# Performance work log

Measured on AMD Instinct MI355X. Metric: run time of the kernel, lower is better.

## Reference

```python
import jax, jax.numpy as jnp
import numpy as np

OUT_FEATURES = 4096
IN_FEATURES = 4096
GROUP_SIZE = 64
N_GROUPS = OUT_FEATURES * IN_FEATURES // GROUP_SIZE  # 262144


def setup_inputs() -> dict:
    key = jax.random.key(0)
    ks = jax.random.split(key, 8)
    x = jax.random.normal(ks[0], (4, 2048, IN_FEATURES), dtype=jnp.float32)
    W_q = jax.random.randint(ks[1], (N_GROUPS, GROUP_SIZE), 0, 16, dtype=jnp.int32)
    scale_q = jax.random.randint(ks[2], (N_GROUPS,), 0, 256, dtype=jnp.int32)
    zero_q = jax.random.randint(ks[3], (N_GROUPS,), 0, 256, dtype=jnp.int32)
    # meta for the nested (quantized) scale / zero: affine params
    s_scale = jax.random.uniform(ks[4], (1,), dtype=jnp.float32) * 1e-3 + 1e-4
    z_scale = jax.random.uniform(ks[5], (1,), dtype=jnp.float32) * 8.0
    s_zero = jax.random.uniform(ks[6], (1,), dtype=jnp.float32) * 0.1 + 1e-3
    z_zero = jax.random.uniform(ks[7], (1,), dtype=jnp.float32) * 8.0
    bias = jax.random.normal(jax.random.fold_in(key, 99), (OUT_FEATURES,), dtype=jnp.float32)
    return {"x": x, "W_q": W_q, "scale_q": scale_q, "zero_q": zero_q,
            "s_scale": s_scale, "z_scale": z_scale,
            "s_zero": s_zero, "z_zero": z_zero, "bias": bias}


def _dequantize(W_q, scale_q, zero_q, s_scale, z_scale, s_zero, z_zero):
    # Nested dequant: scale/zero are themselves 8-bit quantized (HQQ quant_scale/quant_zero)
    scale = (scale_q.astype(jnp.float32) - z_scale) * s_scale      # [n_groups]
    zero = (zero_q.astype(jnp.float32) - z_zero) * s_zero          # [n_groups]
    # per-group affine dequant of the 4-bit weight, then reshape to [out, in]
    W = (W_q.astype(jnp.float32) - zero[:, None]) * scale[:, None]
    return W.reshape(OUT_FEATURES, IN_FEATURES)


def reference(x, W_q, scale_q, zero_q, s_scale, z_scale, s_zero, z_zero, bias):
    W = _dequantize(W_q, scale_q, zero_q, s_scale, z_scale, s_zero, z_zero)
    # forward_pytorch: out = x @ W.T + bias
    out = jnp.einsum("bsi,oi->bso", x, W) + bias
    return out
```

## Files before the change

kernel.cpp:

```cpp
#include <hip/hip_runtime.h>
#include <hip/hip_bf16.h>

#define IN_F 4096
#define OUT_F 4096
#define M_ROWS 8192

#define BM 256
#define BN 256
#define BK 64
#define NT 64

typedef __attribute__((ext_vector_type(8))) __bf16 bf16x8;
typedef __attribute__((ext_vector_type(4))) float f32x4;
typedef __attribute__((address_space(1))) const unsigned int GUI;
typedef __attribute__((address_space(3))) unsigned int LUI;

__global__ __launch_bounds__(256) void dequant_w_kernel(
    const int* __restrict__ Wq, const int* __restrict__ sq, const int* __restrict__ zq,
    const float* __restrict__ ss, const float* __restrict__ zs,
    const float* __restrict__ sz, const float* __restrict__ zz,
    unsigned short* __restrict__ Wb)
{
    int tid = blockIdx.x * blockDim.x + threadIdx.x;
    int g = tid >> 3;
    int off = (tid & 7) << 3;

    float scale = ((float)sq[g] - zs[0]) * ss[0];
    float zero  = ((float)zq[g] - zz[0]) * sz[0];

    const int4* p = reinterpret_cast<const int4*>(Wq + ((size_t)g << 6) + off);
    int4 q0 = p[0], q1 = p[1];
    int qs[8] = {q0.x, q0.y, q0.z, q0.w, q1.x, q1.y, q1.z, q1.w};

    unsigned short w[8];
#pragma unroll
    for (int j = 0; j < 8; ++j) {
        __hip_bfloat16 b = __float2bfloat16(((float)qs[j] - zero) * scale);
        w[j] = *reinterpret_cast<unsigned short*>(&b);
    }
    *reinterpret_cast<int4*>(Wb + ((size_t)g << 6) + off) =
        *reinterpret_cast<int4*>(w);
}

__global__ __launch_bounds__(256) void convert_x_kernel(
    const float* __restrict__ x, unsigned short* __restrict__ xb)
{
    size_t tid = (size_t)blockIdx.x * blockDim.x + threadIdx.x;
    size_t base = tid << 3;
    const float4* p = reinterpret_cast<const float4*>(x + base);
    float4 f0 = p[0], f1 = p[1];
    float fs[8] = {f0.x, f0.y, f0.z, f0.w, f1.x, f1.y, f1.z, f1.w};
    unsigned short w[8];
#pragma unroll
    for (int j = 0; j < 8; ++j) {
        __hip_bfloat16 b = __float2bfloat16(fs[j]);
        w[j] = *reinterpret_cast<unsigned short*>(&b);
    }
    *reinterpret_cast<int4*>(xb + base) = *reinterpret_cast<int4*>(w);
}

__global__ __launch_bounds__(512, 2) void gemm_bf16_kernel(
    const unsigned short* __restrict__ A,
    const unsigned short* __restrict__ B,
    const float* __restrict__ bias,
    float* __restrict__ C)
{
    __shared__ __align__(16) char lds[131072];

    const int K = IN_F;

    int bid = blockIdx.x;
    int swz = (bid & 7) * 64 + (bid >> 3);
    int bx = swz & 15;
    int by = swz >> 4;

    int tid = threadIdx.x;
    int lane = tid & 63;
    int wid = tid >> 6;
    int wr = wid >> 2;
    int wc = wid & 3;

    int roff = tid >> 3;
    int soff = (((tid & 7) ^ ((tid >> 3) & 7)) << 3);
    const unsigned short* srcA = A + (size_t)(by * BM + roff) * K + soff;
    const unsigned short* srcB = B + (size_t)(bx * BN + roff) * K + soff;

#define STAGE_A(kt, h, D2) do {                                               \
    __builtin_amdgcn_global_load_lds(                                         \
        (GUI*)(srcA + (size_t)((h)*128) * IN_F + (size_t)(kt) * BK),          \
        (LUI*)(lds + (D2)*32768 + (h)*16384 + wid*1024), 16, 0, 0);           \
    __builtin_amdgcn_global_load_lds(                                         \
        (GUI*)(srcA + (size_t)((h)*128 + 64) * IN_F + (size_t)(kt) * BK),     \
        (LUI*)(lds + (D2)*32768 + (h)*16384 + 8192 + wid*1024), 16, 0, 0);    \
    } while (0)
#define STAGE_B(kt, h, D2) do {                                               \
    __builtin_amdgcn_global_load_lds(                                         \
        (GUI*)(srcB + (size_t)((h)*128) * IN_F + (size_t)(kt) * BK),          \
        (LUI*)(lds + 65536 + (D2)*32768 + (h)*16384 + wid*1024), 16, 0, 0);   \
    __builtin_amdgcn_global_load_lds(                                         \
        (GUI*)(srcB + (size_t)((h)*128 + 64) * IN_F + (size_t)(kt) * BK),     \
        (LUI*)(lds + 65536 + (D2)*32768 + (h)*16384 + 8192 + wid*1024),       \
        16, 0, 0);                                                            \
    } while (0)

    int lr = lane & 15;
    int kq = lane >> 4;
    int cslot = (kq ^ (lr & 3)) << 4;
    int offk0 = ((lr >> 2) & 1) << 6;
    int offk1 = 64 - offk0;
    int aRd = (wr * 128 + lr) * 128 + cslot;
    int bRd = (wc * 64 + lr) * 128 + cslot;

#define RDA(D2, h, m, ks) (*(const bf16x8*)(lds + (D2)*32768 + aRd +          \
        (h)*8192 + (m)*2048 + ((ks) ? offk1 : offk0)))
#define RDB(D2, c, n, ks) (*(const bf16x8*)(lds + 65536 + (D2)*32768 + bRd +  \
        (c)*4096 + (n)*2048 + ((ks) ? offk1 : offk0)))

    f32x4 acc[8][4] = {};
    bf16x8 a[4][2], b0[2][2], b1[2][2];

#define FENCE asm volatile("" ::: "memory")
#define WAIT_LGKM asm volatile("s_waitcnt lgkmcnt(0)" ::: "memory")

#define KTILE(kt, D, S01, S23, VM) do {                                       \
     \
    __builtin_amdgcn_s_barrier();                                             \
    _Pragma("unroll") for (int m = 0; m < 4; ++m) {                           \
        a[m][0] = RDA(D, 0, m, 0); a[m][1] = RDA(D, 0, m, 1); }               \
    _Pragma("unroll") for (int n = 0; n < 2; ++n) {                           \
        b0[n][0] = RDB(D, 0, n, 0); b0[n][1] = RDB(D, 0, n, 1); }             \
    WAIT_LGKM;                                                                \
    __builtin_amdgcn_s_setprio(1);                                            \
    _Pragma("unroll") for (int m = 0; m < 4; ++m)                             \
    _Pragma("unroll") for (int n = 0; n < 2; ++n)                             \
    _Pragma("unroll") for (int ks = 0; ks < 2; ++ks)                          \
        acc[m][n] = __builtin_amdgcn_mfma_f32_16x16x32_bf16(                  \
            a[m][ks], b0[n][ks], acc[m][n], 0, 0, 0);                         \
    __builtin_amdgcn_s_setprio(0);                                            \
                                    \
    _Pragma("unroll") for (int n = 0; n < 2; ++n) {                           \
        b1[n][0] = RDB(D, 1, n, 0); b1[n][1] = RDB(D, 1, n, 1); }             \
    if (S01) STAGE_B((kt) + 1, 1, (D) ^ 1);                                   \
    FENCE;                                                                    \
     \
    __builtin_amdgcn_s_barrier();                                             \
    WAIT_LGKM;                                                                \
    __builtin_amdgcn_s_setprio(1);                                            \
    _Pragma("unroll") for (int m = 0; m < 4; ++m)                             \
    _Pragma("unroll") for (int n = 0; n < 2; ++n)                             \
    _Pragma("unroll") for (int ks = 0; ks < 2; ++ks)                          \
        acc[m][2 + n] = __builtin_amdgcn_mfma_f32_16x16x32_bf16(              \
            a[m][ks], b1[n][ks], acc[m][2 + n], 0, 0, 0);                     \
    __builtin_amdgcn_s_setprio(0);                                            \
            \
    _Pragma("unroll") for (int m = 0; m < 4; ++m) {                           \
        a[m][0] = RDA(D, 1, m, 0); a[m][1] = RDA(D, 1, m, 1); }               \
    if (S01) STAGE_A((kt) + 1, 1, (D) ^ 1);                                   \
    FENCE;                                                                    \
     \
    __builtin_amdgcn_s_barrier();                                             \
    WAIT_LGKM;                                                                \
    __builtin_amdgcn_s_setprio(1);                                            \
    _Pragma("unroll") for (int m = 0; m < 4; ++m)                             \
    _Pragma("unroll") for (int n = 0; n < 2; ++n)                             \
    _Pragma("unroll") for (int ks = 0; ks < 2; ++ks)                          \
        acc[4 + m][n] = __builtin_amdgcn_mfma_f32_16x16x32_bf16(              \
            a[m][ks], b0[n][ks], acc[4 + m][n], 0, 0, 0);                     \
    __builtin_amdgcn_s_setprio(0);                                            \
                                                  \
    if (S23) STAGE_B((kt) + 2, 0, D);                                         \
    FENCE;                                                                    \
     \
    __builtin_amdgcn_s_barrier();                                             \
    __builtin_amdgcn_s_setprio(1);                                            \
    _Pragma("unroll") for (int m = 0; m < 4; ++m)                             \
    _Pragma("unroll") for (int n = 0; n < 2; ++n)                             \
    _Pragma("unroll") for (int ks = 0; ks < 2; ++ks)                          \
        acc[4 + m][2 + n] = __builtin_amdgcn_mfma_f32_16x16x32_bf16(          \
            a[m][ks], b1[n][ks], acc[4 + m][2 + n], 0, 0, 0);                 \
    __builtin_amdgcn_s_setprio(0);                                            \
                                   \
    if (S23) STAGE_A((kt) + 2, 0, D);                                         \
    if ((VM) == 4) asm volatile("s_waitcnt vmcnt(4)" ::: "memory");           \
    else if ((VM) == 0) asm volatile("s_waitcnt vmcnt(0)" ::: "memory");      \
    FENCE;                                                                    \
    } while (0)

    STAGE_B(0, 0, 0); STAGE_A(0, 0, 0);
    STAGE_B(0, 1, 0); STAGE_A(0, 1, 0);
    STAGE_B(1, 0, 1); STAGE_A(1, 0, 1);
    asm volatile("s_waitcnt vmcnt(4)" ::: "memory");

    for (int t = 0; t < (NT - 2) / 2; ++t) {
        KTILE(2 * t, 0, 1, 1, 4);
        KTILE(2 * t + 1, 1, 1, 1, 4);
    }
    KTILE(NT - 2, 0, 1, 0, 0);
    KTILE(NT - 1, 1, 0, 0, -1);

    int row0 = by * BM + wr * 128 + (lane >> 4) * 4;
    int col0 = bx * BN + wc * 64 + lr;
#pragma unroll
    for (int c = 0; c < 2; ++c)
#pragma unroll
    for (int n = 0; n < 2; ++n) {
        int col = col0 + c * 32 + n * 16;
        float bv = bias[col];
#pragma unroll
        for (int h = 0; h < 2; ++h)
#pragma unroll
        for (int m = 0; m < 4; ++m)
#pragma unroll
        for (int r = 0; r < 4; ++r) {
            int row = row0 + h * 64 + m * 16 + r;
            C[(size_t)row * OUT_F + col] = acc[h * 4 + m][c * 2 + n][r] + bv;
        }
    }
#undef KTILE
#undef FENCE
#undef WAIT_LGKM
#undef RDA
#undef RDB
#undef STAGE_A
#undef STAGE_B
}

extern "C" void kernel_launch(void* const* d_in, const int* in_sizes, int n_in,
                              void* d_out, int out_size, void* d_ws, size_t ws_size,
                              hipStream_t stream) {
    const float* x      = (const float*)d_in[0];
    const int*   Wq     = (const int*)d_in[1];
    const int*   sq     = (const int*)d_in[2];
    const int*   zq     = (const int*)d_in[3];
    const float* ss     = (const float*)d_in[4];
    const float* zs     = (const float*)d_in[5];
    const float* sz     = (const float*)d_in[6];
    const float* zz     = (const float*)d_in[7];
    const float* bias   = (const float*)d_in[8];
    float* out = (float*)d_out;

    unsigned short* xb = (unsigned short*)d_ws;
    unsigned short* Wb = (unsigned short*)((char*)d_ws + (size_t)M_ROWS * IN_F * 2);

    dequant_w_kernel<<<8192, 256, 0, stream>>>(Wq, sq, zq, ss, zs, sz, zz, Wb);
    convert_x_kernel<<<16384, 256, 0, stream>>>(x, xb);
    gemm_bf16_kernel<<<512, 512, 0, stream>>>(xb, Wb, bias, out);
}
```

Baseline: 258.9 us.

## Switch GEMM inner loop from 16x16x32 to 32x32x16 bf16 MFMA tiles

Replaces the 16x16x32 MFMA fragments with 32x32x16 MFMA, reorganising LDS read addressing, per-warp fragment registers, accumulator layout and the epilogue store mapping. Larger MFMA tiles mean fewer LDS fragment reads per FLOP and fewer MFMA issues. The trade-off is the new swizzled read pattern and 16-element accumulators, which change register pressure and may introduce LDS bank conflicts. It also adds an explicit barrier after the prologue.

New measurement: 289.5 us. 11.9% more time.

```diff
diff --git a/kernel.cpp b/kernel.cpp
--- a/kernel.cpp
+++ b/kernel.cpp
@@ -11,7 +11,7 @@
 #define NT 64
 
 typedef __attribute__((ext_vector_type(8))) __bf16 bf16x8;
-typedef __attribute__((ext_vector_type(4))) float f32x4;
+typedef __attribute__((ext_vector_type(16))) float f32x16;
 typedef __attribute__((address_space(1))) const unsigned int GUI;
 typedef __attribute__((address_space(3))) unsigned int LUI;
 
@@ -103,83 +103,83 @@
         16, 0, 0);                                                            \
     } while (0)
 
-    int lr = lane & 15;
-    int kq = lane >> 4;
-    int cslot = (kq ^ (lr & 3)) << 4;
-    int offk0 = ((lr >> 2) & 1) << 6;
-    int offk1 = 64 - offk0;
-    int aRd = (wr * 128 + lr) * 128 + cslot;
-    int bRd = (wc * 64 + lr) * 128 + cslot;
-
-#define RDA(D2, h, m, ks) (*(const bf16x8*)(lds + (D2)*32768 + aRd +          \
-        (h)*8192 + (m)*2048 + ((ks) ? offk1 : offk0)))
-#define RDB(D2, c, n, ks) (*(const bf16x8*)(lds + 65536 + (D2)*32768 + bRd +  \
-        (c)*4096 + (n)*2048 + ((ks) ? offk1 : offk0)))
-
-    f32x4 acc[8][4] = {};
-    bf16x8 a[4][2], b0[2][2], b1[2][2];
+    int l31 = lane & 31;
+    int kgrp = lane >> 5;
+    int sb[4];
+#pragma unroll
+    for (int ks = 0; ks < 4; ++ks)
+        sb[ks] = (((ks * 2 + kgrp) ^ (lane & 7)) << 4);
+    int aBase = wr * 16384 + l31 * 128;
+    int bBase = (wc >> 1) * 16384 + ((wc & 1) * 64 + l31) * 128;
+
+#define RA(D2, mb, ks) (*(const bf16x8*)(lds + (D2)*32768 + aBase +           \
+        (mb)*4096 + sb[ks]))
+#define RB(D2, nb, ks) (*(const bf16x8*)(lds + 65536 + (D2)*32768 + bBase +   \
+        (nb)*4096 + sb[ks]))
+
+    f32x16 acc[4][2] = {};
+    bf16x8 aF[2][4], bF0[4], bF1[4];
 
 #define FENCE asm volatile("" ::: "memory")
 #define WAIT_LGKM asm volatile("s_waitcnt lgkmcnt(0)" ::: "memory")
+#define BARRIER asm volatile("s_barrier" ::: "memory")
 
 #define KTILE(kt, D, S01, S23, VM) do {                                       \
      \
-    __builtin_amdgcn_s_barrier();                                             \
-    _Pragma("unroll") for (int m = 0; m < 4; ++m) {                           \
-        a[m][0] = RDA(D, 0, m, 0); a[m][1] = RDA(D, 0, m, 1); }               \
-    _Pragma("unroll") for (int n = 0; n < 2; ++n) {                           \
-        b0[n][0] = RDB(D, 0, n, 0); b0[n][1] = RDB(D, 0, n, 1); }             \
+    BARRIER;                                                                  \
+    _Pragma("unroll") for (int q = 0; q < 2; ++q)                             \
+    _Pragma("unroll") for (int ks = 0; ks < 4; ++ks)                          \
+        aF[q][ks] = RA(D, q, ks);                                             \
+    _Pragma("unroll") for (int ks = 0; ks < 4; ++ks)                          \
+        bF0[ks] = RB(D, 0, ks);                                               \
     WAIT_LGKM;                                                                \
     __builtin_amdgcn_s_setprio(1);                                            \
-    _Pragma("unroll") for (int m = 0; m < 4; ++m)                             \
-    _Pragma("unroll") for (int n = 0; n < 2; ++n)                             \
-    _Pragma("unroll") for (int ks = 0; ks < 2; ++ks)                          \
-        acc[m][n] = __builtin_amdgcn_mfma_f32_16x16x32_bf16(                  \
-            a[m][ks], b0[n][ks], acc[m][n], 0, 0, 0);                         \
-    __builtin_amdgcn_s_setprio(0);                                            \
-                                    \
-    _Pragma("unroll") for (int n = 0; n < 2; ++n) {                           \
-        b1[n][0] = RDB(D, 1, n, 0); b1[n][1] = RDB(D, 1, n, 1); }             \
+    _Pragma("unroll") for (int q = 0; q < 2; ++q)                             \
+    _Pragma("unroll") for (int ks = 0; ks < 4; ++ks)                          \
+        acc[q][0] = __builtin_amdgcn_mfma_f32_32x32x16_bf16(                  \
+            aF[q][ks], bF0[ks], acc[q][0], 0, 0, 0);                          \
+    __builtin_amdgcn_s_setprio(0);                                            \
+                                   \
+    _Pragma("unroll") for (int ks = 0; ks < 4; ++ks)                          \
+        bF1[ks] = RB(D, 1, ks);                                               \
     if (S01) STAGE_B((kt) + 1, 1, (D) ^ 1);                                   \
     FENCE;                                                                    \
      \
-    __builtin_amdgcn_s_barrier();                                             \
+    BARRIER;                                                                  \
     WAIT_LGKM;                                                                \
     __builtin_amdgcn_s_setprio(1);                                            \
-    _Pragma("unroll") for (int m = 0; m < 4; ++m)                             \
-    _Pragma("unroll") for (int n = 0; n < 2; ++n)                             \
-    _Pragma("unroll") for (int ks = 0; ks < 2; ++ks)                          \
-        acc[m][2 + n] = __builtin_amdgcn_mfma_f32_16x16x32_bf16(              \
-            a[m][ks], b1[n][ks], acc[m][2 + n], 0, 0, 0);                     \
-    __builtin_amdgcn_s_setprio(0);                                            \
-            \
-    _Pragma("unroll") for (int m = 0; m < 4; ++m) {                           \
-        a[m][0] = RDA(D, 1, m, 0); a[m][1] = RDA(D, 1, m, 1); }               \
+    _Pragma("unroll") for (int q = 0; q < 2; ++q)                             \
+    _Pragma("unroll") for (int ks = 0; ks < 4; ++ks)                          \
+        acc[q][1] = __builtin_amdgcn_mfma_f32_32x32x16_bf16(                  \
+            aF[q][ks], bF1[ks], acc[q][1], 0, 0, 0);                          \
+    __builtin_amdgcn_s_setprio(0);                                            \
+               \
+    _Pragma("unroll") for (int q = 0; q < 2; ++q)                             \
+    _Pragma("unroll") for (int ks = 0; ks < 4; ++ks)                          \
+        aF[q][ks] = RA(D, 2 + q, ks);                                         \
     if (S01) STAGE_A((kt) + 1, 1, (D) ^ 1);                                   \
     FENCE;                                                                    \
      \
-    __builtin_amdgcn_s_barrier();                                             \
+    BARRIER;                                                                  \
     WAIT_LGKM;                                                                \
     __builtin_amdgcn_s_setprio(1);                                            \
-    _Pragma("unroll") for (int m = 0; m < 4; ++m)                             \
-    _Pragma("unroll") for (int n = 0; n < 2; ++n)                             \
-    _Pragma("unroll") for (int ks = 0; ks < 2; ++ks)                          \
-        acc[4 + m][n] = __builtin_amdgcn_mfma_f32_16x16x32_bf16(              \
-            a[m][ks], b0[n][ks], acc[4 + m][n], 0, 0, 0);                     \
-    __builtin_amdgcn_s_setprio(0);                                            \
-                                                  \
+    _Pragma("unroll") for (int q = 0; q < 2; ++q)                             \
+    _Pragma("unroll") for (int ks = 0; ks < 4; ++ks)                          \
+        acc[2 + q][0] = __builtin_amdgcn_mfma_f32_32x32x16_bf16(              \
+            aF[q][ks], bF0[ks], acc[2 + q][0], 0, 0, 0);                      \
+    __builtin_amdgcn_s_setprio(0);                                            \
+                                                 \
     if (S23) STAGE_B((kt) + 2, 0, D);                                         \
     FENCE;                                                                    \
      \
-    __builtin_amdgcn_s_barrier();                                             \
-    __builtin_amdgcn_s_setprio(1);                                            \
-    _Pragma("unroll") for (int m = 0; m < 4; ++m)                             \
-    _Pragma("unroll") for (int n = 0; n < 2; ++n)                             \
-    _Pragma("unroll") for (int ks = 0; ks < 2; ++ks)                          \
-        acc[4 + m][2 + n] = __builtin_amdgcn_mfma_f32_16x16x32_bf16(          \
-            a[m][ks], b1[n][ks], acc[4 + m][2 + n], 0, 0, 0);                 \
-    __builtin_amdgcn_s_setprio(0);                                            \
-                                   \
+    BARRIER;                                                                  \
+    __builtin_amdgcn_s_setprio(1);                                            \
+    _Pragma("unroll") for (int q = 0; q < 2; ++q)                             \
+    _Pragma("unroll") for (int ks = 0; ks < 4; ++ks)                          \
+        acc[2 + q][1] = __builtin_amdgcn_mfma_f32_32x32x16_bf16(              \
+            aF[q][ks], bF1[ks], acc[2 + q][1], 0, 0, 0);                      \
+    __builtin_amdgcn_s_setprio(0);                                            \
+                                  \
     if (S23) STAGE_A((kt) + 2, 0, D);                                         \
     if ((VM) == 4) asm volatile("s_waitcnt vmcnt(4)" ::: "memory");           \
     else if ((VM) == 0) asm volatile("s_waitcnt vmcnt(0)" ::: "memory");      \
@@ -190,6 +190,7 @@
     STAGE_B(0, 1, 0); STAGE_A(0, 1, 0);
     STAGE_B(1, 0, 1); STAGE_A(1, 0, 1);
     asm volatile("s_waitcnt vmcnt(4)" ::: "memory");
+    BARRIER;
 
     for (int t = 0; t < (NT - 2) / 2; ++t) {
         KTILE(2 * t, 0, 1, 1, 4);
@@ -198,29 +199,27 @@
     KTILE(NT - 2, 0, 1, 0, 0);
     KTILE(NT - 1, 1, 0, 0, -1);
 
-    int row0 = by * BM + wr * 128 + (lane >> 4) * 4;
-    int col0 = bx * BN + wc * 64 + lr;
-#pragma unroll
-    for (int c = 0; c < 2; ++c)
-#pragma unroll
-    for (int n = 0; n < 2; ++n) {
-        int col = col0 + c * 32 + n * 16;
+    int colBase = bx * BN + wc * 64 + l31;
+    int rowBase = by * BM + wr * 128 + 4 * kgrp;
+#pragma unroll
+    for (int nb = 0; nb < 2; ++nb) {
+        int col = colBase + nb * 32;
         float bv = bias[col];
 #pragma unroll
-        for (int h = 0; h < 2; ++h)
-#pragma unroll
-        for (int m = 0; m < 4; ++m)
-#pragma unroll
-        for (int r = 0; r < 4; ++r) {
-            int row = row0 + h * 64 + m * 16 + r;
-            C[(size_t)row * OUT_F + col] = acc[h * 4 + m][c * 2 + n][r] + bv;
+        for (int mb = 0; mb < 4; ++mb) {
+#pragma unroll
+            for (int r = 0; r < 16; ++r) {
+                int row = rowBase + mb * 32 + (r & 3) + 8 * (r >> 2);
+                C[(size_t)row * OUT_F + col] = acc[mb][nb][r] + bv;
+            }
         }
     }
 #undef KTILE
 #undef FENCE
 #undef WAIT_LGKM
-#undef RDA
-#undef RDB
+#undef BARRIER
+#undef RA
+#undef RB
 #undef STAGE_A
 #undef STAGE_B
 }
```
